# Performance work log

Hardware: AMD Instinct MI355X
Metric: run time of the kernel (lower is better)

The kernel has to match this reference:

```python
import jax, jax.numpy as jnp
import numpy as np

N, C, H, W = 8, 256, 31, 31
HIDDEN, OUT = 512, 256


def setup_inputs() -> dict:
    key = jax.random.key(0)
    k0, k1, k2, k3, k4 = jax.random.split(key, 5)
    x = jax.random.normal(k0, (N, C, H, W), dtype=jnp.float32)
    # Linear params (torch nn.Linear layout: [out_features, in_features])
    W1 = jax.random.normal(k1, (HIDDEN, C), dtype=jnp.float32) * (1.0 / np.sqrt(C))
    b1 = jax.random.normal(k2, (HIDDEN,), dtype=jnp.float32) * 0.01
    W2 = jax.random.normal(k3, (OUT, HIDDEN), dtype=jnp.float32) * (1.0 / np.sqrt(HIDDEN))
    b2 = jax.random.normal(k4, (OUT,), dtype=jnp.float32) * 0.01
    return {"x": x, "W1": W1, "b1": b1, "W2": W2, "b2": b2}


def _normalized_adjacency(n, h, w):
    M = n * h * w
    idx = jnp.arange(M)
    blk = idx // (h * w)          # sample id of each node
    pos = idx % (h * w)           # spatial position within sample
    # block-diagonal all-ones per sample
    same_block = (blk[:, None] == blk[None, :]).astype(jnp.float32)
    # identity link between consecutive samples (disjoint from block-diag)
    neighbor = ((jnp.abs(blk[:, None] - blk[None, :]) == 1)
                & (pos[:, None] == pos[None, :])).astype(jnp.float32)
    A = same_block + neighbor + jnp.eye(M, dtype=jnp.float32)
    deg = A.sum(axis=1)
    dinv = jnp.where(deg > 0, deg ** -0.5, 0.0)
    return A * dinv[:, None] * dinv[None, :]  # D^-1/2 A D^-1/2


def reference(x, W1, b1, W2, b2):
    n, c, h, w = x.shape
    weight = _normalized_adjacency(n, h, w)                 # [M, M]
    nodes = x.transpose(0, 2, 3, 1).reshape(-1, c)          # [M, C]
    hid = jax.nn.leaky_relu(weight @ nodes @ W1.T + b1)     # [M, HIDDEN]
    hid = jax.nn.leaky_relu(weight @ hid @ W2.T + b2)       # [M, OUT]
    hid = hid.reshape(n, h, w, -1).transpose(0, 3, 1, 2)    # [N, OUT, H, W]
    return hid.max(axis=0, keepdims=True)                   # [1, OUT, H, W]
```

## Files before the change

kernel.cpp:

```cpp
#include <hip/hip_runtime.h>
#include <math.h>

#define NS   8
#define CC   256
#define PP   961
#define MM   7688
#define MP   7744
#define HID  512
#define OUTC 256

typedef _Float16 h16;
using half8   = __attribute__((ext_vector_type(8))) _Float16;
using floatx4 = __attribute__((ext_vector_type(4))) float;

#define AS1 __attribute__((address_space(1)))
#define AS3 __attribute__((address_space(3)))

__device__ __forceinline__ float dinv_of(int b) {
    return (b == 0 || b == NS - 1) ? 0.0322245515f : 0.0322078318f;
}

__global__ void prep(const float* __restrict__ W1, const float* __restrict__ W2,
                     h16* __restrict__ w1h, h16* __restrict__ w2h,
                     const float* __restrict__ x, h16* __restrict__ Xt,
                     float* __restrict__ SZ, float* __restrict__ SY) {
    int blk = blockIdx.x, tid = threadIdx.x;
    if (blk < 256) {
        bool second = blk >= 128;
        const float* src = second ? W2 : W1;
        h16* dst = second ? w2h : w1h;
        int i = ((blk & 127) * 256 + tid) * 4;
        float4 v = *(const float4*)(src + i);
        dst[i + 0] = (h16)v.x; dst[i + 1] = (h16)v.y;
        dst[i + 2] = (h16)v.z; dst[i + 3] = (h16)v.w;
    } else if (blk < 2240) {
        __shared__ h16 tr[32][33];
        int t = blk - 256;
        int b = t & 7, ct = (t >> 3) & 7, pt = t >> 6;
        int p0 = pt * 32, c0 = ct * 32;
        int j = tid & 31, i0 = tid >> 5;
        int p = p0 + j;
        #pragma unroll
        for (int r = 0; r < 4; ++r) {
            int c = c0 + i0 + r * 8;
            float v = (p < PP) ? x[((size_t)b * CC + c) * PP + p] : 0.f;
            tr[i0 + r * 8][j] = (h16)v;
        }
        __syncthreads();
        #pragma unroll
        for (int r = 0; r < 4; ++r) {
            int ii = tid & 31;
            int jj = (tid >> 5) + r * 8;
            int pw = p0 + jj;
            if (pw < PP)
                Xt[((size_t)b * PP + pw) * CC + c0 + ii] = tr[ii][jj];
        }
    } else {
        int i = (blk - 2240) * 256 + tid;
        if (i < NS * HID) SZ[i] = 0.f;
        else SY[i - NS * HID] = 0.f;
    }
}

template<int KD, bool ACT, bool DO_SUM, typename OutT>
__global__ __launch_bounds__(256) void mfma_gemm(
    const h16* __restrict__ A,
    const h16* __restrict__ B,
    const float* __restrict__ bias,
    OutT* __restrict__ C,
    float* __restrict__ S,
    int M, int Nc)
{
    __shared__ __align__(16) h16 As[64 * 64];
    __shared__ __align__(16) h16 Bs[64 * 64];
    int tid = threadIdx.x, wave = tid >> 6, lane = tid & 63;
    int m0 = blockIdx.x * 64, n0 = blockIdx.y * 64;
    int sro = lane >> 3;
    int sch = (lane & 7) ^ sro;
    const h16* ga0 = A + (size_t)(m0 + wave * 16 + sro) * KD + sch * 8;
    const h16* gb0 = B + (size_t)(n0 + wave * 16 + sro) * KD + sch * 8;
    h16* la0 = &As[(wave * 16) * 64];
    h16* la1 = &As[(wave * 16 + 8) * 64];
    h16* lb0 = &Bs[(wave * 16) * 64];
    h16* lb1 = &Bs[(wave * 16 + 8) * 64];
    int fr = lane & 15, fq = lane >> 4;
    floatx4 acc[4] = {{0.f,0.f,0.f,0.f},{0.f,0.f,0.f,0.f},{0.f,0.f,0.f,0.f},{0.f,0.f,0.f,0.f}};
    for (int kk = 0; kk < KD; kk += 64) {
        __builtin_amdgcn_global_load_lds((const AS1 void*)(const void*)(ga0 + kk),
                                         (AS3 void*)(void*)la0, 16, 0, 0);
        __builtin_amdgcn_global_load_lds((const AS1 void*)(const void*)(ga0 + 8 * KD + kk),
                                         (AS3 void*)(void*)la1, 16, 0, 0);
        __builtin_amdgcn_global_load_lds((const AS1 void*)(const void*)(gb0 + kk),
                                         (AS3 void*)(void*)lb0, 16, 0, 0);
        __builtin_amdgcn_global_load_lds((const AS1 void*)(const void*)(gb0 + 8 * KD + kk),
                                         (AS3 void*)(void*)lb1, 16, 0, 0);
        __syncthreads();
        #pragma unroll
        for (int ks = 0; ks < 2; ++ks) {
            int slot = (ks * 4 + fq) ^ (fr & 7);
            half8 bf = *(const half8*)&Bs[(wave * 16 + fr) * 64 + slot * 8];
            #pragma unroll
            for (int mb = 0; mb < 4; ++mb) {
                half8 af = *(const half8*)&As[(mb * 16 + fr) * 64 + slot * 8];
                acc[mb] = __builtin_amdgcn_mfma_f32_16x16x32_f16(af, bf, acc[mb], 0, 0, 0);
            }
        }
        __syncthreads();
    }
    int col = n0 + wave * 16 + fr;
    float bv = ACT ? bias[col] : 0.f;
    float s_lo = 0.f, s_hi = 0.f;
    int blo = m0 / 961;
    int mcut = (blo + 1) * 961;
    #pragma unroll
    for (int mb = 0; mb < 4; ++mb) {
        #pragma unroll
        for (int r = 0; r < 4; ++r) {
            int m = m0 + mb * 16 + fq * 4 + r;
            if (m < M) {
                float v = acc[mb][r] + bv;
                if (ACT) v = (v >= 0.f) ? v : 0.01f * v;
                C[(size_t)m * Nc + col] = (OutT)v;
                if (DO_SUM) { if (m < mcut) s_lo += v; else s_hi += v; }
            }
        }
    }
    if (DO_SUM) {
        s_lo += __shfl_xor(s_lo, 16);
        s_lo += __shfl_xor(s_lo, 32);
        s_hi += __shfl_xor(s_hi, 16);
        s_hi += __shfl_xor(s_hi, 32);
        if (fq == 0) {
            atomicAdd(&S[blo * Nc + col], s_lo);
            int bhi = (m0 + 63) / 961;
            if (bhi != blo && bhi < NS) atomicAdd(&S[bhi * Nc + col], s_hi);
        }
    }
}

__global__ __launch_bounds__(256) void gemm2_fused(
    const h16* __restrict__ Z,
    const h16* __restrict__ B,
    const float* __restrict__ SZ,
    const float* __restrict__ b1v,
    float* __restrict__ C,
    float* __restrict__ SY)
{
    __shared__ __align__(16) h16 Zc[64 * 64];
    __shared__ __align__(16) h16 Zm[64 * 64];
    __shared__ __align__(16) h16 Zp[64 * 64];
    __shared__ __align__(16) h16 Hs[64 * 64];
    __shared__ __align__(16) h16 Bs[64 * 64];
    int tid = threadIdx.x, wave = tid >> 6, lane = tid & 63;
    int m0 = blockIdx.x * 64, n0 = blockIdx.y * 64;
    int sro = lane >> 3;
    int sch = (lane & 7) ^ sro;
    const h16* gzc = Z + (ptrdiff_t)(m0 + wave * 16 + sro) * HID + sch * 8;
    const h16* gzm = gzc - (ptrdiff_t)PP * HID;
    const h16* gzp = gzc + (ptrdiff_t)PP * HID;
    const h16* gbb = B + (size_t)(n0 + wave * 16 + sro) * HID + sch * 8;
    h16* lzc0 = &Zc[(wave * 16) * 64];     h16* lzc1 = &Zc[(wave * 16 + 8) * 64];
    h16* lzm0 = &Zm[(wave * 16) * 64];     h16* lzm1 = &Zm[(wave * 16 + 8) * 64];
    h16* lzp0 = &Zp[(wave * 16) * 64];     h16* lzp1 = &Zp[(wave * 16 + 8) * 64];
    h16* lb0  = &Bs[(wave * 16) * 64];     h16* lb1  = &Bs[(wave * 16 + 8) * 64];
    int fr = lane & 15, fq = lane >> 4;
    int hr = tid >> 2;
    int hc0 = (tid & 3) * 2;
    int hm = m0 + hr;
    int hb = hm / PP; if (hb > NS - 1) hb = NS - 1;
    float db = dinv_of(hb);
    float dm = (hb > 0)      ? db * dinv_of(hb - 1) : 0.f;
    float dp = (hb < NS - 1) ? db * dinv_of(hb + 1) : 0.f;
    float db2 = db * db;
    floatx4 acc[4] = {{0.f,0.f,0.f,0.f},{0.f,0.f,0.f,0.f},{0.f,0.f,0.f,0.f},{0.f,0.f,0.f,0.f}};
    for (int kk = 0; kk < HID; kk += 64) {
        __builtin_amdgcn_global_load_lds((const AS1 void*)(const void*)(gzc + kk),
                                         (AS3 void*)(void*)lzc0, 16, 0, 0);
        __builtin_amdgcn_global_load_lds((const AS1 void*)(const void*)(gzc + 8 * HID + kk),
                                         (AS3 void*)(void*)lzc1, 16, 0, 0);
        __builtin_amdgcn_global_load_lds((const AS1 void*)(const void*)(gzm + kk),
                                         (AS3 void*)(void*)lzm0, 16, 0, 0);
        __builtin_amdgcn_global_load_lds((const AS1 void*)(const void*)(gzm + 8 * HID + kk),
                                         (AS3 void*)(void*)lzm1, 16, 0, 0);
        __builtin_amdgcn_global_load_lds((const AS1 void*)(const void*)(gzp + kk),
                                         (AS3 void*)(void*)lzp0, 16, 0, 0);
        __builtin_amdgcn_global_load_lds((const AS1 void*)(const void*)(gzp + 8 * HID + kk),
                                         (AS3 void*)(void*)lzp1, 16, 0, 0);
        __builtin_amdgcn_global_load_lds((const AS1 void*)(const void*)(gbb + kk),
                                         (AS3 void*)(void*)lb0, 16, 0, 0);
        __builtin_amdgcn_global_load_lds((const AS1 void*)(const void*)(gbb + 8 * HID + kk),
                                         (AS3 void*)(void*)lb1, 16, 0, 0);
        __syncthreads();
        #pragma unroll
        for (int qi = 0; qi < 2; ++qi) {
            int ch = hc0 + qi;
            int slot = ch ^ (hr & 7);
            int off = hr * 64 + slot * 8;
            half8 zc = *(const half8*)&Zc[off];
            half8 zm = *(const half8*)&Zm[off];
            half8 zp = *(const half8*)&Zp[off];
            int h0 = kk + ch * 8;
            float4 s0  = *(const float4*)(SZ + hb * HID + h0);
            float4 s1  = *(const float4*)(SZ + hb * HID + h0 + 4);
            float4 bb0 = *(const float4*)(b1v + h0);
            float4 bb1 = *(const float4*)(b1v + h0 + 4);
            float ss[8] = {s0.x, s0.y, s0.z, s0.w, s1.x, s1.y, s1.z, s1.w};
            float bb[8] = {bb0.x, bb0.y, bb0.z, bb0.w, bb1.x, bb1.y, bb1.z, bb1.w};
            half8 o;
            #pragma unroll
            for (int j = 0; j < 8; ++j) {
                float v = db2 * (ss[j] + (float)zc[j])
                        + dm * (float)zm[j] + dp * (float)zp[j] + bb[j];
                v = (v >= 0.f) ? v : 0.01f * v;
                o[j] = (h16)v;
            }
            *(half8*)&Hs[off] = o;
        }
        __syncthreads();
        #pragma unroll
        for (int ks = 0; ks < 2; ++ks) {
            int slot = (ks * 4 + fq) ^ (fr & 7);
            half8 bf = *(const half8*)&Bs[(wave * 16 + fr) * 64 + slot * 8];
            #pragma unroll
            for (int mb = 0; mb < 4; ++mb) {
                half8 af = *(const half8*)&Hs[(mb * 16 + fr) * 64 + slot * 8];
                acc[mb] = __builtin_amdgcn_mfma_f32_16x16x32_f16(af, bf, acc[mb], 0, 0, 0);
            }
        }
        __syncthreads();
    }
    int col = n0 + wave * 16 + fr;
    float s_lo = 0.f, s_hi = 0.f;
    int blo = m0 / 961;
    int mcut = (blo + 1) * 961;
    #pragma unroll
    for (int mb = 0; mb < 4; ++mb) {
        #pragma unroll
        for (int r = 0; r < 4; ++r) {
            int m = m0 + mb * 16 + fq * 4 + r;
            if (m < MM) {
                float v = acc[mb][r];
                C[(size_t)m * OUTC + col] = v;
                if (m < mcut) s_lo += v; else s_hi += v;
            }
        }
    }
    s_lo += __shfl_xor(s_lo, 16);
    s_lo += __shfl_xor(s_lo, 32);
    s_hi += __shfl_xor(s_hi, 16);
    s_hi += __shfl_xor(s_hi, 32);
    if (fq == 0) {
        atomicAdd(&SY[blo * OUTC + col], s_lo);
        int bhi = (m0 + 63) / 961;
        if (bhi != blo && bhi < NS) atomicAdd(&SY[bhi * OUTC + col], s_hi);
    }
}

__global__ void final_max(const float* __restrict__ Y, const float* __restrict__ SY,
                          const float* __restrict__ b2, float* __restrict__ out) {
    int pt = blockIdx.x, ot = blockIdx.y;
    int p0 = pt * 32, o0 = ot * 32;
    __shared__ float t[32][33];
    int i = threadIdx.x & 31, j0 = threadIdx.x >> 5;
    int o = o0 + i;
    float bias = b2[o];
    #pragma unroll
    for (int r = 0; r < 4; ++r) {
        int j = j0 + r * 8;
        int p = p0 + j;
        float vmax = -INFINITY;
        if (p < PP) {
            float y[NS];
            #pragma unroll
            for (int b = 0; b < NS; ++b)
                y[b] = Y[((size_t)b * PP + p) * OUTC + o];
            #pragma unroll
            for (int b = 0; b < NS; ++b) {
                float db = dinv_of(b);
                float a = db * (SY[b * OUTC + o] + y[b]);
                if (b > 0)      a += dinv_of(b - 1) * y[b - 1];
                if (b < NS - 1) a += dinv_of(b + 1) * y[b + 1];
                float z = db * a + bias;
                z = (z >= 0.f) ? z : 0.01f * z;
                vmax = fmaxf(vmax, z);
            }
        }
        t[j][i] = vmax;
    }
    __syncthreads();
    int jj = threadIdx.x & 31, ii0 = threadIdx.x >> 5;
    #pragma unroll
    for (int r = 0; r < 4; ++r) {
        int ii = ii0 + r * 8;
        int pw = p0 + jj;
        if (pw < PP)
            out[(size_t)(o0 + ii) * PP + pw] = t[jj][ii];
    }
}

extern "C" void kernel_launch(void* const* d_in, const int* in_sizes, int n_in,
                              void* d_out, int out_size, void* d_ws, size_t ws_size,
                              hipStream_t stream) {
    const float* x  = (const float*)d_in[0];
    const float* W1 = (const float*)d_in[1];
    const float* b1 = (const float*)d_in[2];
    const float* W2 = (const float*)d_in[3];
    const float* b2 = (const float*)d_in[4];
    float* out = (float*)d_out;
    float* ws  = (float*)d_ws;

    float* SZ  = ws;
    float* SY  = ws + 4096;
    h16*  w1h  = (h16*)(ws + 6144);
    h16*  w2h  = (h16*)(ws + 71680);
    h16*  Xt   = (h16*)(ws + 137216);
    h16*  Zbuf = (h16*)(ws + 1128448);
    h16*  Z    = Zbuf + (size_t)1024 * HID;
    float* Y   = ws + 3635200;

    prep<<<2264, 256, 0, stream>>>(W1, W2, w1h, w2h, x, Xt, SZ, SY);
    mfma_gemm<CC, false, true, h16><<<dim3(MP / 64, HID / 64), 256, 0, stream>>>(
        Xt, w1h, nullptr, Z, SZ, MM, HID);
    gemm2_fused<<<dim3(MP / 64, OUTC / 64), 256, 0, stream>>>(Z, w2h, SZ, b1, Y, SY);
    final_max<<<dim3(31, 8), 256, 0, stream>>>(Y, SY, b2, out);
}
```

Baseline: 101.6 us.

## Interleave Z and Y rows by sample so gemm2 tiles hold all neighbors

Gemm1 now writes Z in a permuted row order in which each 64-row tile holds 8 spatial positions across all 8 samples. Gemm2 can then build the adjacency-mixed hidden tile from a single Z tile in LDS, replacing three separate loads of the current, previous and next sample tiles. Final_max reads Y in the same permuted layout. The goal is to cut global and LDS traffic in gemm2. In exchange, gemm1 stores become scattered, and padded rows must be masked to zero.

```diff
diff --git a/kernel.cpp b/kernel.cpp
--- a/kernel.cpp
+++ b/kernel.cpp
@@ -18,6 +18,10 @@
 
 __device__ __forceinline__ float dinv_of(int b) {
     return (b == 0 || b == NS - 1) ? 0.0322245515f : 0.0322078318f;
+}
+
+__device__ __forceinline__ int rho_of(int b, int p) {
+    return ((p >> 3) << 6) + (b << 3) + (p & 7);
 }
 
 __global__ void prep(const float* __restrict__ W1, const float* __restrict__ W2,
@@ -62,14 +66,11 @@
     }
 }
 
-template<int KD, bool ACT, bool DO_SUM, typename OutT>
-__global__ __launch_bounds__(256) void mfma_gemm(
+__global__ __launch_bounds__(256) void gemm1(
     const h16* __restrict__ A,
     const h16* __restrict__ B,
-    const float* __restrict__ bias,
-    OutT* __restrict__ C,
-    float* __restrict__ S,
-    int M, int Nc)
+    h16* __restrict__ Z,
+    float* __restrict__ SZ)
 {
     __shared__ __align__(16) h16 As[64 * 64];
     __shared__ __align__(16) h16 Bs[64 * 64];
@@ -77,22 +78,22 @@
     int m0 = blockIdx.x * 64, n0 = blockIdx.y * 64;
     int sro = lane >> 3;
     int sch = (lane & 7) ^ sro;
-    const h16* ga0 = A + (size_t)(m0 + wave * 16 + sro) * KD + sch * 8;
-    const h16* gb0 = B + (size_t)(n0 + wave * 16 + sro) * KD + sch * 8;
+    const h16* ga0 = A + (size_t)(m0 + wave * 16 + sro) * CC + sch * 8;
+    const h16* gb0 = B + (size_t)(n0 + wave * 16 + sro) * CC + sch * 8;
     h16* la0 = &As[(wave * 16) * 64];
     h16* la1 = &As[(wave * 16 + 8) * 64];
     h16* lb0 = &Bs[(wave * 16) * 64];
     h16* lb1 = &Bs[(wave * 16 + 8) * 64];
     int fr = lane & 15, fq = lane >> 4;
     floatx4 acc[4] = {{0.f,0.f,0.f,0.f},{0.f,0.f,0.f,0.f},{0.f,0.f,0.f,0.f},{0.f,0.f,0.f,0.f}};
-    for (int kk = 0; kk < KD; kk += 64) {
+    for (int kk = 0; kk < CC; kk += 64) {
         __builtin_amdgcn_global_load_lds((const AS1 void*)(const void*)(ga0 + kk),
                                          (AS3 void*)(void*)la0, 16, 0, 0);
-        __builtin_amdgcn_global_load_lds((const AS1 void*)(const void*)(ga0 + 8 * KD + kk),
+        __builtin_amdgcn_global_load_lds((const AS1 void*)(const void*)(ga0 + 8 * CC + kk),
                                          (AS3 void*)(void*)la1, 16, 0, 0);
         __builtin_amdgcn_global_load_lds((const AS1 void*)(const void*)(gb0 + kk),
                                          (AS3 void*)(void*)lb0, 16, 0, 0);
-        __builtin_amdgcn_global_load_lds((const AS1 void*)(const void*)(gb0 + 8 * KD + kk),
+        __builtin_amdgcn_global_load_lds((const AS1 void*)(const void*)(gb0 + 8 * CC + kk),
                                          (AS3 void*)(void*)lb1, 16, 0, 0);
         __syncthreads();
         #pragma unroll
@@ -108,7 +109,6 @@
         __syncthreads();
     }
     int col = n0 + wave * 16 + fr;
-    float bv = ACT ? bias[col] : 0.f;
     float s_lo = 0.f, s_hi = 0.f;
     int blo = m0 / 961;
     int mcut = (blo + 1) * 961;
@@ -117,88 +117,77 @@
         #pragma unroll
         for (int r = 0; r < 4; ++r) {
             int m = m0 + mb * 16 + fq * 4 + r;
-            if (m < M) {
-                float v = acc[mb][r] + bv;
-                if (ACT) v = (v >= 0.f) ? v : 0.01f * v;
-                C[(size_t)m * Nc + col] = (OutT)v;
-                if (DO_SUM) { if (m < mcut) s_lo += v; else s_hi += v; }
-            }
-        }
-    }
-    if (DO_SUM) {
-        s_lo += __shfl_xor(s_lo, 16);
-        s_lo += __shfl_xor(s_lo, 32);
-        s_hi += __shfl_xor(s_hi, 16);
-        s_hi += __shfl_xor(s_hi, 32);
-        if (fq == 0) {
-            atomicAdd(&S[blo * Nc + col], s_lo);
-            int bhi = (m0 + 63) / 961;
-            if (bhi != blo && bhi < NS) atomicAdd(&S[bhi * Nc + col], s_hi);
-        }
-    }
-}
-
-__global__ __launch_bounds__(256) void gemm2_fused(
+            if (m < MM) {
+                float v = acc[mb][r];
+                int b = m / 961;
+                int p = m - b * 961;
+                Z[(size_t)rho_of(b, p) * HID + col] = (h16)v;
+                if (m < mcut) s_lo += v; else s_hi += v;
+            }
+        }
+    }
+    s_lo += __shfl_xor(s_lo, 16);
+    s_lo += __shfl_xor(s_lo, 32);
+    s_hi += __shfl_xor(s_hi, 16);
+    s_hi += __shfl_xor(s_hi, 32);
+    if (fq == 0) {
+        atomicAdd(&SZ[blo * HID + col], s_lo);
+        int bhi = (m0 + 63) / 961;
+        if (bhi != blo && bhi < NS) atomicAdd(&SZ[bhi * HID + col], s_hi);
+    }
+}
+
+__global__ __launch_bounds__(256) void gemm2_rho(
     const h16* __restrict__ Z,
     const h16* __restrict__ B,
     const float* __restrict__ SZ,
     const float* __restrict__ b1v,
-    float* __restrict__ C,
+    float* __restrict__ Y,
     float* __restrict__ SY)
 {
-    __shared__ __align__(16) h16 Zc[64 * 64];
-    __shared__ __align__(16) h16 Zm[64 * 64];
-    __shared__ __align__(16) h16 Zp[64 * 64];
+    __shared__ __align__(16) h16 Zs[64 * 64];
     __shared__ __align__(16) h16 Hs[64 * 64];
     __shared__ __align__(16) h16 Bs[64 * 64];
     int tid = threadIdx.x, wave = tid >> 6, lane = tid & 63;
-    int m0 = blockIdx.x * 64, n0 = blockIdx.y * 64;
+    int rt = blockIdx.x;
+    int n0 = blockIdx.y * 64;
     int sro = lane >> 3;
     int sch = (lane & 7) ^ sro;
-    const h16* gzc = Z + (ptrdiff_t)(m0 + wave * 16 + sro) * HID + sch * 8;
-    const h16* gzm = gzc - (ptrdiff_t)PP * HID;
-    const h16* gzp = gzc + (ptrdiff_t)PP * HID;
-    const h16* gbb = B + (size_t)(n0 + wave * 16 + sro) * HID + sch * 8;
-    h16* lzc0 = &Zc[(wave * 16) * 64];     h16* lzc1 = &Zc[(wave * 16 + 8) * 64];
-    h16* lzm0 = &Zm[(wave * 16) * 64];     h16* lzm1 = &Zm[(wave * 16 + 8) * 64];
-    h16* lzp0 = &Zp[(wave * 16) * 64];     h16* lzp1 = &Zp[(wave * 16 + 8) * 64];
-    h16* lb0  = &Bs[(wave * 16) * 64];     h16* lb1  = &Bs[(wave * 16 + 8) * 64];
+    const h16* gz0 = Z + (size_t)(rt * 64 + wave * 16 + sro) * HID + sch * 8;
+    const h16* gb0 = B + (size_t)(n0 + wave * 16 + sro) * HID + sch * 8;
+    h16* lz0 = &Zs[(wave * 16) * 64];
+    h16* lz1 = &Zs[(wave * 16 + 8) * 64];
+    h16* lb0 = &Bs[(wave * 16) * 64];
+    h16* lb1 = &Bs[(wave * 16 + 8) * 64];
     int fr = lane & 15, fq = lane >> 4;
     int hr = tid >> 2;
     int hc0 = (tid & 3) * 2;
-    int hm = m0 + hr;
-    int hb = hm / PP; if (hb > NS - 1) hb = NS - 1;
-    float db = dinv_of(hb);
-    float dm = (hb > 0)      ? db * dinv_of(hb - 1) : 0.f;
-    float dp = (hb < NS - 1) ? db * dinv_of(hb + 1) : 0.f;
+    int hb = hr >> 3;
+    bool pvalid = (rt * 8 + (hr & 7)) < PP;
+    float db  = dinv_of(hb);
+    float dmw = (hb > 0)      ? db * dinv_of(hb - 1) : 0.f;
+    float dpw = (hb < NS - 1) ? db * dinv_of(hb + 1) : 0.f;
     float db2 = db * db;
+    int hrm = (hb > 0)      ? hr - 8 : hr;
+    int hrp = (hb < NS - 1) ? hr + 8 : hr;
     floatx4 acc[4] = {{0.f,0.f,0.f,0.f},{0.f,0.f,0.f,0.f},{0.f,0.f,0.f,0.f},{0.f,0.f,0.f,0.f}};
     for (int kk = 0; kk < HID; kk += 64) {
-        __builtin_amdgcn_global_load_lds((const AS1 void*)(const void*)(gzc + kk),
-                                         (AS3 void*)(void*)lzc0, 16, 0, 0);
-        __builtin_amdgcn_global_load_lds((const AS1 void*)(const void*)(gzc + 8 * HID + kk),
-                                         (AS3 void*)(void*)lzc1, 16, 0, 0);
-        __builtin_amdgcn_global_load_lds((const AS1 void*)(const void*)(gzm + kk),
-                                         (AS3 void*)(void*)lzm0, 16, 0, 0);
-        __builtin_amdgcn_global_load_lds((const AS1 void*)(const void*)(gzm + 8 * HID + kk),
-                                         (AS3 void*)(void*)lzm1, 16, 0, 0);
-        __builtin_amdgcn_global_load_lds((const AS1 void*)(const void*)(gzp + kk),
-                                         (AS3 void*)(void*)lzp0, 16, 0, 0);
-        __builtin_amdgcn_global_load_lds((const AS1 void*)(const void*)(gzp + 8 * HID + kk),
-                                         (AS3 void*)(void*)lzp1, 16, 0, 0);
-        __builtin_amdgcn_global_load_lds((const AS1 void*)(const void*)(gbb + kk),
+        __builtin_amdgcn_global_load_lds((const AS1 void*)(const void*)(gz0 + kk),
+                                         (AS3 void*)(void*)lz0, 16, 0, 0);
+        __builtin_amdgcn_global_load_lds((const AS1 void*)(const void*)(gz0 + 8 * HID + kk),
+                                         (AS3 void*)(void*)lz1, 16, 0, 0);
+        __builtin_amdgcn_global_load_lds((const AS1 void*)(const void*)(gb0 + kk),
                                          (AS3 void*)(void*)lb0, 16, 0, 0);
-        __builtin_amdgcn_global_load_lds((const AS1 void*)(const void*)(gbb + 8 * HID + kk),
+        __builtin_amdgcn_global_load_lds((const AS1 void*)(const void*)(gb0 + 8 * HID + kk),
                                          (AS3 void*)(void*)lb1, 16, 0, 0);
         __syncthreads();
         #pragma unroll
         for (int qi = 0; qi < 2; ++qi) {
             int ch = hc0 + qi;
             int slot = ch ^ (hr & 7);
-            int off = hr * 64 + slot * 8;
-            half8 zc = *(const half8*)&Zc[off];
-            half8 zm = *(const half8*)&Zm[off];
-            half8 zp = *(const half8*)&Zp[off];
+            half8 zc = *(const half8*)&Zs[hr  * 64 + slot * 8];
+            half8 zm = *(const half8*)&Zs[hrm * 64 + slot * 8];
+            half8 zp = *(const half8*)&Zs[hrp * 64 + slot * 8];
             int h0 = kk + ch * 8;
             float4 s0  = *(const float4*)(SZ + hb * HID + h0);
             float4 s1  = *(const float4*)(SZ + hb * HID + h0 + 4);
@@ -210,11 +199,11 @@
             #pragma unroll
             for (int j = 0; j < 8; ++j) {
                 float v = db2 * (ss[j] + (float)zc[j])
-                        + dm * (float)zm[j] + dp * (float)zp[j] + bb[j];
+                        + dmw * (float)zm[j] + dpw * (float)zp[j] + bb[j];
                 v = (v >= 0.f) ? v : 0.01f * v;
-                o[j] = (h16)v;
-            }
-            *(half8*)&Hs[off] = o;
+                o[j] = pvalid ? (h16)v : (h16)0.f;
+            }
+            *(half8*)&Hs[hr * 64 + slot * 8] = o;
         }
         __syncthreads();
         #pragma unroll
@@ -230,29 +219,27 @@
         __syncthreads();
     }
     int col = n0 + wave * 16 + fr;
-    float s_lo = 0.f, s_hi = 0.f;
-    int blo = m0 / 961;
-    int mcut = (blo + 1) * 961;
+    size_t row0 = (size_t)rt * 64;
+    float sb[4];
     #pragma unroll
     for (int mb = 0; mb < 4; ++mb) {
+        float s = 0.f;
         #pragma unroll
         for (int r = 0; r < 4; ++r) {
-            int m = m0 + mb * 16 + fq * 4 + r;
-            if (m < MM) {
-                float v = acc[mb][r];
-                C[(size_t)m * OUTC + col] = v;
-                if (m < mcut) s_lo += v; else s_hi += v;
-            }
-        }
-    }
-    s_lo += __shfl_xor(s_lo, 16);
-    s_lo += __shfl_xor(s_lo, 32);
-    s_hi += __shfl_xor(s_hi, 16);
-    s_hi += __shfl_xor(s_hi, 32);
-    if (fq == 0) {
-        atomicAdd(&SY[blo * OUTC + col], s_lo);
-        int bhi = (m0 + 63) / 961;
-        if (bhi != blo && bhi < NS) atomicAdd(&SY[bhi * OUTC + col], s_hi);
+            int row = 16 * mb + 4 * fq + r;
+            float v = acc[mb][r];
+            Y[(row0 + row) * OUTC + col] = v;
+            s += v;
+        }
+        sb[mb] = s;
+    }
+    #pragma unroll
+    for (int mb = 0; mb < 4; ++mb) sb[mb] += __shfl_xor(sb[mb], 16);
+    if (fq == 0 || fq == 2) {
+        int bodd = (fq >= 2) ? 1 : 0;
+        #pragma unroll
+        for (int mb = 0; mb < 4; ++mb)
+            atomicAdd(&SY[(2 * mb + bodd) * OUTC + col], sb[mb]);
     }
 }
 
@@ -270,10 +257,11 @@
         int p = p0 + j;
         float vmax = -INFINITY;
         if (p < PP) {
+            size_t rbase = (size_t)(((p >> 3) << 6) + (p & 7)) * OUTC + o;
             float y[NS];
             #pragma unroll
             for (int b = 0; b < NS; ++b)
-                y[b] = Y[((size_t)b * PP + p) * OUTC + o];
+                y[b] = Y[rbase + (size_t)b * 8 * OUTC];
             #pragma unroll
             for (int b = 0; b < NS; ++b) {
                 float db = dinv_of(b);
@@ -314,13 +302,11 @@
     h16*  w1h  = (h16*)(ws + 6144);
     h16*  w2h  = (h16*)(ws + 71680);
     h16*  Xt   = (h16*)(ws + 137216);
-    h16*  Zbuf = (h16*)(ws + 1128448);
-    h16*  Z    = Zbuf + (size_t)1024 * HID;
-    float* Y   = ws + 3635200;
+    h16*  Z    = (h16*)(ws + 1128448);
+    float* Y   = ws + 3110912;
 
     prep<<<2264, 256, 0, stream>>>(W1, W2, w1h, w2h, x, Xt, SZ, SY);
-    mfma_gemm<CC, false, true, h16><<<dim3(MP / 64, HID / 64), 256, 0, stream>>>(
-        Xt, w1h, nullptr, Z, SZ, MM, HID);
-    gemm2_fused<<<dim3(MP / 64, OUTC / 64), 256, 0, stream>>>(Z, w2h, SZ, b1, Y, SY);
+    gemm1<<<dim3(MP / 64, HID / 64), 256, 0, stream>>>(Xt, w1h, Z, SZ);
+    gemm2_rho<<<dim3(MP / 64, OUTC / 64), 256, 0, stream>>>(Z, w2h, SZ, b1, Y, SY);
     final_max<<<dim3(31, 8), 256, 0, stream>>>(Y, SY, b2, out);
 }
```

New measurement: 102.8 us. No clear change (+1.2%).
